# Kernel optimization log

Hardware: AMD Instinct MI355X
Metric: run time of the kernel (lower is better)

The kernel has to match this reference:

```python
import jax, jax.numpy as jnp
import numpy as np

B, S = 4, 2048
DM, H, DK, DV, DI = 512, 4, 128, 128, 1024
NT, NV = 64, 5000
PAD = 0


def layernorm(x, g, b, eps=1e-5):
    m = jnp.mean(x, axis=-1, keepdims=True)
    v = jnp.var(x, axis=-1, keepdims=True)
    return (x - m) * jax.lax.rsqrt(v + eps) * g + b


def setup_inputs() -> dict:
    key = jax.random.key(0)
    ks = jax.random.split(key, 20)
    event_type = jax.random.randint(ks[0], (B, S), 0, NT + 1)
    vertex = jax.random.randint(ks[1], (B, S), 0, NV + 1)
    vertex = jnp.where(event_type == PAD, 0, vertex)  # align padding
    event_time = jnp.sort(jax.random.uniform(ks[2], (B, S)) * 100.0, axis=1)
    non_pad_mask = (event_type != PAD).astype(jnp.float32)[..., None]  # [B,S,1]
    sc = 0.02
    event_emb = jax.random.normal(ks[3], (NT + 1, DM)) * sc
    event_emb = event_emb.at[PAD].set(0.0)
    vertex_emb = jax.random.normal(ks[4], (NV + 1, DM)) * sc
    vertex_emb = vertex_emb.at[PAD].set(0.0)
    A = jax.random.uniform(ks[5], (NV, NV))
    W = jax.random.uniform(ks[6], (NV, NV))
    Wq = jax.random.normal(ks[7], (DM, H * DK)) * sc
    Wk = jax.random.normal(ks[8], (DM, H * DK)) * sc
    Wv = jax.random.normal(ks[9], (DM, H * DV)) * sc
    Wo = jax.random.normal(ks[10], (H * DV, DM)) * sc
    bo = jnp.zeros((DM,))
    ln1_g, ln1_b = jnp.ones((DM,)), jnp.zeros((DM,))
    w1 = jax.random.normal(ks[11], (DM, DI)) * sc
    b1 = jnp.zeros((DI,))
    w2 = jax.random.normal(ks[12], (DI, DM)) * sc
    b2 = jnp.zeros((DM,))
    ln2_g, ln2_b = jnp.ones((DM,)), jnp.zeros((DM,))
    return dict(event_type=event_type, vertex=vertex, event_time=event_time,
                non_pad_mask=non_pad_mask, A=A, W=W, event_emb=event_emb,
                vertex_emb=vertex_emb, Wq=Wq, Wk=Wk, Wv=Wv, Wo=Wo, bo=bo,
                ln1_g=ln1_g, ln1_b=ln1_b, w1=w1, b1=b1, w2=w2, b2=b2,
                ln2_g=ln2_g, ln2_b=ln2_b)


def similarity(vertex, A, W):
    # vectorized form of the triple-loop pairwise gather: [B,1,S,S]
    idx = jnp.clip(vertex - 1, 0)                       # [B,S]
    vm = (vertex != 0)
    pair = vm[:, :, None] & vm[:, None, :]              # [B,S,S]
    sim = A[idx[:, :, None], idx[:, None, :]] * W[idx[:, :, None], idx[:, None, :]] * 10.0
    return (sim * pair.astype(A.dtype))[:, None]        # [B,1,S,S]


def temporal_enc(event_time, non_pad_mask, d_model):
    i = jnp.arange(d_model)
    pv = jnp.power(jnp.float32(10000.0), 2.0 * (i // 2).astype(jnp.float32) / d_model)
    r = event_time[:, :, None] / pv                     # [B,S,D]
    return jnp.where(i % 2 == 0, jnp.sin(r), jnp.cos(r)) * non_pad_mask


def reference(event_type, vertex, event_time, non_pad_mask, A, W, event_emb,
              vertex_emb, Wq, Wk, Wv, Wo, bo, ln1_g, ln1_b, w1, b1, w2, b2,
              ln2_g, ln2_b):
    b_, s_ = event_type.shape
    # masks: key-padding OR subsequent (causal)
    pad = (event_type == PAD)
    subseq = jnp.triu(jnp.ones((s_, s_), dtype=bool), 1)
    slf_attn_mask = pad[:, None, :] | subseq[None]      # [B,S,S]

    sim = similarity(vertex, A, W)                      # [B,1,S,S]
    tem = temporal_enc(event_time, non_pad_mask, DM)    # [B,S,D]
    ver = vertex_emb[vertex]                            # [B,S,D]
    enc = event_emb[event_type]                         # [B,S,D]

    # single encoder layer (n_layers=1), post-norm THP-style
    enc = enc + ver + tem
    res = enc
    q = (enc @ Wq).reshape(b_, s_, H, DK)
    k = (enc @ Wk).reshape(b_, s_, H, DK)
    v = (enc @ Wv).reshape(b_, s_, H, DV)
    scores = jnp.einsum('bihd,bjhd->bhij', q, k) / jnp.sqrt(jnp.float32(DK)) + sim
    scores = jnp.where(slf_attn_mask[:, None], jnp.float32(-1e9), scores)
    attn = jax.nn.softmax(scores, axis=-1)
    o = jnp.einsum('bhij,bjhd->bihd', attn, v).reshape(b_, s_, H * DV)
    o = o @ Wo + bo
    enc = layernorm(o + res, ln1_g, ln1_b) * non_pad_mask
    res = enc
    f = jax.nn.relu(enc @ w1 + b1) @ w2 + b2
    enc = layernorm(f + res, ln2_g, ln2_b) * non_pad_mask
    return enc, sim
```

## Files before the change

### kernel.cpp

```cpp
#include <hip/hip_runtime.h>
#include <hip/hip_bf16.h>

#define B_ 4
#define S_ 2048
#define DM_ 512
#define H_ 4
#define DK_ 128
#define DI_ 1024
#define NV_ 5000

typedef __attribute__((ext_vector_type(8))) short bf16x8;
typedef __attribute__((ext_vector_type(8))) unsigned short u16x8;
typedef __attribute__((ext_vector_type(4))) unsigned short u16x4;
typedef __attribute__((ext_vector_type(4))) float f32x4;

__device__ inline unsigned short f2bf(float x) {
  unsigned int u = __float_as_uint(x);
  unsigned int r = (u + 0x7fffu + ((u >> 16) & 1u)) >> 16;
  return (unsigned short)r;
}
__device__ inline float bf2f(unsigned short u) {
  return __uint_as_float(((unsigned int)u) << 16);
}
__device__ inline void gload16(const void* g, void* l) {
  __builtin_amdgcn_global_load_lds(
      (const __attribute__((address_space(1))) void*)g,
      (__attribute__((address_space(3))) void*)l, 16, 0, 0);
}

__global__ __launch_bounds__(256) void embed_kernel(
    const int* __restrict__ et, const int* __restrict__ vx,
    const float* __restrict__ tmv, const float* __restrict__ npm,
    const float* __restrict__ eemb, const float* __restrict__ vemb,
    float* __restrict__ enc0, unsigned short* __restrict__ enc0b) {
  int row = blockIdx.x;
  int t = et[row], v = vx[row];
  float time = tmv[row], mask = npm[row];
  int tid = threadIdx.x;
  #pragma unroll
  for (int k = 0; k < 2; ++k) {
    int dd = tid + k * 256;
    float pv = powf(10000.0f, (float)(dd & ~1) / 512.0f);
    float r = time / pv;
    float tem = (((dd & 1) == 0) ? sinf(r) : cosf(r)) * mask;
    float val = eemb[(size_t)t * DM_ + dd] + vemb[(size_t)v * DM_ + dd] + tem;
    enc0[(size_t)row * DM_ + dd] = val;
    enc0b[(size_t)row * DM_ + dd] = f2bf(val);
  }
}

__global__ __launch_bounds__(256) void sim_kernel(
    const int* __restrict__ vx, const float* __restrict__ A,
    const float* __restrict__ W, float* __restrict__ sim) {
  __shared__ float Ar[NV_];
  __shared__ float Wr[NV_];
  int i = blockIdx.x;
  int b = blockIdx.y;
  int vi = vx[b * S_ + i];
  float* out = sim + ((size_t)(b * S_ + i)) * S_;
  int tid = threadIdx.x;
  if (vi == 0) {
    for (int j = tid * 4; j < S_; j += 1024)
      *(float4*)&out[j] = (float4){0.f, 0.f, 0.f, 0.f};
    return;
  }
  const float4* Arow = (const float4*)(A + (size_t)(vi - 1) * NV_);
  const float4* Wrow = (const float4*)(W + (size_t)(vi - 1) * NV_);
  for (int j = tid; j < NV_ / 4; j += 256) {
    ((float4*)Ar)[j] = Arow[j];
    ((float4*)Wr)[j] = Wrow[j];
  }
  __syncthreads();
  for (int j = tid * 4; j < S_; j += 1024) {
    int4 vj = *(const int4*)&vx[b * S_ + j];
    float4 o;
    o.x = vj.x ? Ar[vj.x - 1] * Wr[vj.x - 1] * 10.0f : 0.f;
    o.y = vj.y ? Ar[vj.y - 1] * Wr[vj.y - 1] * 10.0f : 0.f;
    o.z = vj.z ? Ar[vj.z - 1] * Wr[vj.z - 1] * 10.0f : 0.f;
    o.w = vj.w ? Ar[vj.w - 1] * Wr[vj.w - 1] * 10.0f : 0.f;
    *(float4*)&out[j] = o;
  }
}

__global__ __launch_bounds__(256) void wt_kernel(
    const float* __restrict__ W, unsigned short* __restrict__ WT,
    int K, int N) {
  __shared__ unsigned short T[32][40];
  int n0 = blockIdx.x * 32, k0 = blockIdx.y * 32;
  int r = threadIdx.x >> 3, c0 = (threadIdx.x & 7) * 4;
  float4 v = *(const float4*)&W[(size_t)(k0 + r) * N + n0 + c0];
  T[r][c0 + 0] = f2bf(v.x);
  T[r][c0 + 1] = f2bf(v.y);
  T[r][c0 + 2] = f2bf(v.z);
  T[r][c0 + 3] = f2bf(v.w);
  __syncthreads();
  u16x4 o;
  o[0] = T[c0 + 0][r]; o[1] = T[c0 + 1][r];
  o[2] = T[c0 + 2][r]; o[3] = T[c0 + 3][r];
  *(u16x4*)&WT[(size_t)(n0 + r) * K + k0 + c0] = o;
}

template <int OMODE, bool RELU>
__global__ __launch_bounds__(256) void gemm_bf16_kernel(
    const unsigned short* __restrict__ A, const unsigned short* __restrict__ BT,
    const float* __restrict__ bias, void* __restrict__ C,
    int M, int N, int K) {
  __shared__ __attribute__((aligned(16))) unsigned short As[128][72];
  __shared__ __attribute__((aligned(16))) unsigned short Bs[128][72];
  int tid = threadIdx.x;
  int w = tid >> 6, l = tid & 63;
  int l16 = l & 15, lh = l >> 4;
  int wr = w >> 1, wc = w & 1;
  int row0 = blockIdx.y * 128, col0 = blockIdx.x * 128;
  int ra = tid >> 1, ha = (tid & 1) * 32;
  f32x4 acc[4][4];
  #pragma unroll
  for (int m = 0; m < 4; ++m)
    #pragma unroll
    for (int n = 0; n < 4; ++n) acc[m][n] = (f32x4){0.f, 0.f, 0.f, 0.f};

  for (int k0 = 0; k0 < K; k0 += 64) {
    __syncthreads();
    {
      const unsigned short* sa = &A[(size_t)(row0 + ra) * K + k0 + ha];
      uint4 a0 = *(const uint4*)(sa);
      uint4 a1 = *(const uint4*)(sa + 8);
      uint4 a2 = *(const uint4*)(sa + 16);
      uint4 a3 = *(const uint4*)(sa + 24);
      *(uint4*)&As[ra][ha + 0] = a0;
      *(uint4*)&As[ra][ha + 8] = a1;
      *(uint4*)&As[ra][ha + 16] = a2;
      *(uint4*)&As[ra][ha + 24] = a3;
      const unsigned short* sb = &BT[(size_t)(col0 + ra) * K + k0 + ha];
      uint4 b0 = *(const uint4*)(sb);
      uint4 b1 = *(const uint4*)(sb + 8);
      uint4 b2 = *(const uint4*)(sb + 16);
      uint4 b3 = *(const uint4*)(sb + 24);
      *(uint4*)&Bs[ra][ha + 0] = b0;
      *(uint4*)&Bs[ra][ha + 8] = b1;
      *(uint4*)&Bs[ra][ha + 16] = b2;
      *(uint4*)&Bs[ra][ha + 24] = b3;
    }
    __syncthreads();
    #pragma unroll
    for (int kc = 0; kc < 2; ++kc) {
      bf16x8 af[4], bfr[4];
      #pragma unroll
      for (int m = 0; m < 4; ++m)
        af[m] = *(bf16x8*)&As[wr * 64 + m * 16 + l16][kc * 32 + lh * 8];
      #pragma unroll
      for (int n = 0; n < 4; ++n)
        bfr[n] = *(bf16x8*)&Bs[wc * 64 + n * 16 + l16][kc * 32 + lh * 8];
      #pragma unroll
      for (int m = 0; m < 4; ++m)
        #pragma unroll
        for (int n = 0; n < 4; ++n)
          acc[m][n] = __builtin_amdgcn_mfma_f32_16x16x32_bf16(af[m], bfr[n], acc[m][n], 0, 0, 0);
    }
  }
  #pragma unroll
  for (int m = 0; m < 4; ++m) {
    #pragma unroll
    for (int r = 0; r < 4; ++r) {
      int row = row0 + wr * 64 + m * 16 + lh * 4 + r;
      #pragma unroll
      for (int n = 0; n < 4; ++n) {
        int colg = col0 + wc * 64 + n * 16 + l16;
        float v = acc[m][n][r];
        if (bias) v += bias[colg];
        if (RELU) v = fmaxf(v, 0.f);
        if (OMODE == 0) {
          ((float*)C)[(size_t)row * N + colg] = v;
        } else if (OMODE == 1) {
          ((unsigned short*)C)[(size_t)row * N + colg] = f2bf(v);
        } else {
          int which = colg >> 9;
          int cl = colg & 511;
          int b = row >> 11, s = row & 2047;
          int h = cl >> 7, d = cl & 127;
          unsigned short* base =
              (unsigned short*)C + (size_t)which * (4194304);
          if (which < 2)
            base[((size_t)((b * 4 + h) * 2048 + s)) * 128 + d] = f2bf(v);
          else
            base[((size_t)((b * 4 + h) * 128 + d)) * 2048 + s] = f2bf(v);
        }
      }
    }
  }
}

__global__ __launch_bounds__(256) void attn_mfma_kernel(
    const unsigned short* __restrict__ Qb, const unsigned short* __restrict__ Kb,
    const unsigned short* __restrict__ Vt, const float* __restrict__ sim,
    const float* __restrict__ npm, unsigned short* __restrict__ Op0,
    unsigned short* __restrict__ Op1, float2* __restrict__ ml0,
    float2* __restrict__ ml1) {
  __shared__ __attribute__((aligned(16))) char KsL[2][16384];
  __shared__ __attribute__((aligned(16))) char VtsL[2][16384];
  __shared__ __attribute__((aligned(16))) unsigned short Pl[4][16][72];
  int bid = blockIdx.x;
  int xcd = bid & 7;
  int j0 = bid >> 3;
  int bh = xcd * 2 + (j0 & 1);
  int jj = j0 >> 1;
  int pair = jj & 15;
  int half = jj >> 4;
  int b = bh >> 2;
  int tid = threadIdx.x;
  int w = tid >> 6, l = tid & 63;
  int l16 = l & 15, lh = l >> 4;
  unsigned short* Op = half ? Op1 : Op0;
  float2* ml = half ? ml1 : ml0;

  const char* KbB = (const char*)Kb + (size_t)bh * 2048 * 256;
  const char* VtB = (const char*)Vt + (size_t)bh * 128 * 4096;
  int krow[4], kcol[4], vrow4[4], vcol[4];
  #pragma unroll
  for (int j = 0; j < 4; ++j) {
    int i = w * 4 + j;
    krow[j] = i * 4 + (l >> 4);
    kcol[j] = ((l & 15) * 16) ^ ((krow[j] & 7) << 4);
    vrow4[j] = i * 8 + (l >> 3);
    vcol[j] = ((l & 7) * 16) ^ ((vrow4[j] & 7) << 4);
  }
  int xr = (l16 & 7) << 4;

  #pragma unroll 1
  for (int pj = 0; pj < 2; ++pj) {
    int qt = pj ? 31 - pair : pair;
    int nst = qt + 1;
    int c0 = (nst + 1) >> 1;
    int t0 = half ? c0 : 0;
    int cnt = half ? nst - c0 : c0;
    int q0 = qt * 64 + w * 16;
    int qg = q0 + l16;

    bf16x8 qf[4];
    const unsigned short* Qrow = Qb + ((size_t)(bh * 2048 + qg)) * 128;
    #pragma unroll
    for (int kq = 0; kq < 4; ++kq)
      qf[kq] = *(const bf16x8*)&Qrow[kq * 32 + lh * 8];

    float m_l = -INFINITY, l_l = 0.f;
    f32x4 o_acc[8];
    #pragma unroll
    for (int c = 0; c < 8; ++c) o_acc[c] = (f32x4){0.f, 0.f, 0.f, 0.f};

    const float* simrow = sim + ((size_t)(b * 2048) + qg) * 2048;
    const float* mrow = npm + b * 2048;

    if (cnt > 0) {
      #pragma unroll
      for (int j = 0; j < 4; ++j) {
        int i = w * 4 + j;
        gload16(KbB + (size_t)(t0 * 64 + krow[j]) * 256 + kcol[j],
                &KsL[0][i * 1024]);
        gload16(VtB + (size_t)vrow4[j] * 4096 + (size_t)(t0 * 64) * 2 + vcol[j],
                &VtsL[0][i * 1024]);
      }
      asm volatile("s_waitcnt vmcnt(0)" ::: "memory");
      __syncthreads();

      #pragma unroll 1
      for (int ti = 0; ti < cnt; ++ti) {
        int cur = ti & 1;
        int kv0 = (t0 + ti) * 64;
        if (ti + 1 < cnt) {
          int kvn = kv0 + 64;
          #pragma unroll
          for (int j = 0; j < 4; ++j) {
            int i = w * 4 + j;
            gload16(KbB + (size_t)(kvn + krow[j]) * 256 + kcol[j],
                    &KsL[cur ^ 1][i * 1024]);
            gload16(VtB + (size_t)vrow4[j] * 4096 + (size_t)kvn * 2 + vcol[j],
                    &VtsL[cur ^ 1][i * 1024]);
          }
        }
        const char* Kbase = KsL[cur];
        f32x4 sc[4];
        #pragma unroll
        for (int tt = 0; tt < 4; ++tt) {
          sc[tt] = (f32x4){0.f, 0.f, 0.f, 0.f};
          const char* Krow = Kbase + (tt * 16 + l16) * 256;
          #pragma unroll
          for (int kq = 0; kq < 4; ++kq) {
            bf16x8 kf = *(const bf16x8*)(Krow + ((kq * 64 + lh * 16) ^ xr));
            sc[tt] = __builtin_amdgcn_mfma_f32_16x16x32_bf16(kf, qf[kq], sc[tt], 0, 0, 0);
          }
        }
        float4 sim4[4], mk4[4];
        #pragma unroll
        for (int tt = 0; tt < 4; ++tt) {
          sim4[tt] = *(const float4*)&simrow[kv0 + tt * 16 + lh * 4];
          mk4[tt] = *(const float4*)&mrow[kv0 + tt * 16 + lh * 4];
        }
        float sv[4][4];
        #pragma unroll
        for (int tt = 0; tt < 4; ++tt) {
          #pragma unroll
          for (int r = 0; r < 4; ++r) {
            int kvg = kv0 + tt * 16 + lh * 4 + r;
            float mkr = r == 0 ? mk4[tt].x : r == 1 ? mk4[tt].y
                      : r == 2 ? mk4[tt].z : mk4[tt].w;
            float smr = r == 0 ? sim4[tt].x : r == 1 ? sim4[tt].y
                      : r == 2 ? sim4[tt].z : sim4[tt].w;
            bool valid = (kvg <= qg) && (mkr != 0.f);
            sv[tt][r] = valid ? sc[tt][r] * 0.08838834764831845f + smr : -1e9f;
          }
        }
        float mx = sv[0][0];
        #pragma unroll
        for (int tt = 0; tt < 4; ++tt)
          #pragma unroll
          for (int r = 0; r < 4; ++r) mx = fmaxf(mx, sv[tt][r]);
        mx = fmaxf(mx, __shfl_xor(mx, 16));
        mx = fmaxf(mx, __shfl_xor(mx, 32));
        float mn = fmaxf(m_l, mx);
        float alpha = __expf(m_l - mn);
        m_l = mn;
        float ts = 0.f;
        #pragma unroll
        for (int tt = 0; tt < 4; ++tt)
          #pragma unroll
          for (int r = 0; r < 4; ++r) {
            float ppv = __expf(sv[tt][r] - mn);
            sv[tt][r] = ppv;
            ts += ppv;
          }
        ts += __shfl_xor(ts, 16);
        ts += __shfl_xor(ts, 32);
        l_l = l_l * alpha + ts;
        #pragma unroll
        for (int tt = 0; tt < 4; ++tt) {
          u16x4 pw;
          pw[0] = f2bf(sv[tt][0]); pw[1] = f2bf(sv[tt][1]);
          pw[2] = f2bf(sv[tt][2]); pw[3] = f2bf(sv[tt][3]);
          *(u16x4*)&Pl[w][l16][tt * 16 + lh * 4] = pw;
        }
        float al[4];
        #pragma unroll
        for (int r = 0; r < 4; ++r) al[r] = __shfl(alpha, lh * 4 + r);
        #pragma unroll
        for (int c = 0; c < 8; ++c)
          #pragma unroll
          for (int r = 0; r < 4; ++r) o_acc[c][r] *= al[r];
        const char* Vbase = VtsL[cur];
        #pragma unroll
        for (int kf2 = 0; kf2 < 2; ++kf2) {
          bf16x8 pa = *(bf16x8*)&Pl[w][l16][kf2 * 32 + lh * 8];
          #pragma unroll
          for (int c = 0; c < 8; ++c) {
            bf16x8 vf = *(const bf16x8*)(Vbase + (c * 16 + l16) * 128 +
                                         ((kf2 * 64 + lh * 16) ^ xr));
            o_acc[c] = __builtin_amdgcn_mfma_f32_16x16x32_bf16(pa, vf, o_acc[c], 0, 0, 0);
          }
        }
        asm volatile("s_waitcnt vmcnt(0)" ::: "memory");
        __syncthreads();
      }
    }
    #pragma unroll
    for (int r = 0; r < 4; ++r) {
      int qgr = q0 + lh * 4 + r;
      unsigned short* op = Op + ((size_t)(bh * 2048 + qgr)) * 128;
      #pragma unroll
      for (int c = 0; c < 8; ++c) op[c * 16 + l16] = f2bf(o_acc[c][r]);
    }
    if (lh == 0) {
      float2 v; v.x = m_l; v.y = l_l;
      ml[bh * 2048 + q0 + l16] = v;
    }
    __syncthreads();
  }
}

__global__ __launch_bounds__(256) void attn_combine_kernel(
    const unsigned short* __restrict__ Op0, const unsigned short* __restrict__ Op1,
    const float2* __restrict__ ml0, const float2* __restrict__ ml1,
    unsigned short* __restrict__ Of) {
  int idx = blockIdx.x * 256 + threadIdx.x;
  int row = idx >> 4;
  int d0 = (idx & 15) * 8;
  float2 a = ml0[row], c2 = ml1[row];
  float m = fmaxf(a.x, c2.x);
  float e1 = __expf(a.x - m), e2 = __expf(c2.x - m);
  float inv = 1.f / (e1 * a.y + e2 * c2.y);
  u16x8 o1 = *(const u16x8*)&Op0[(size_t)row * 128 + d0];
  u16x8 o2 = *(const u16x8*)&Op1[(size_t)row * 128 + d0];
  int bh = row >> 11, q = row & 2047;
  int b = bh >> 2, h = bh & 3;
  unsigned short* dst = Of + ((size_t)(b * 2048 + q)) * 512 + h * 128 + d0;
  u16x8 o;
  #pragma unroll
  for (int j = 0; j < 8; ++j)
    o[j] = f2bf((bf2f(o1[j]) * e1 + bf2f(o2[j]) * e2) * inv);
  *(u16x8*)dst = o;
}

__global__ __launch_bounds__(256) void ln_kernel(
    const float* __restrict__ x, const float* __restrict__ res,
    const float* __restrict__ g, const float* __restrict__ bta,
    const float* __restrict__ npm, float* __restrict__ out,
    unsigned short* __restrict__ out16) {
  __shared__ float ssum[4], ssq[4];
  int row = blockIdx.x;
  int tid = threadIdx.x;
  size_t base = (size_t)row * DM_;
  float v0 = x[base + tid] + res[base + tid];
  float v1 = x[base + tid + 256] + res[base + tid + 256];
  float sum = v0 + v1, sq = v0 * v0 + v1 * v1;
  #pragma unroll
  for (int off = 32; off >= 1; off >>= 1) {
    sum += __shfl_down(sum, off);
    sq += __shfl_down(sq, off);
  }
  int wid = tid >> 6, lane = tid & 63;
  if (lane == 0) { ssum[wid] = sum; ssq[wid] = sq; }
  __syncthreads();
  sum = ssum[0] + ssum[1] + ssum[2] + ssum[3];
  sq = ssq[0] + ssq[1] + ssq[2] + ssq[3];
  float mean = sum * (1.f / DM_);
  float var = sq * (1.f / DM_) - mean * mean;
  float rs = rsqrtf(var + 1e-5f);
  float mask = npm[row];
  float o0 = ((v0 - mean) * rs * g[tid] + bta[tid]) * mask;
  float o1 = ((v1 - mean) * rs * g[tid + 256] + bta[tid + 256]) * mask;
  out[base + tid] = o0;
  out[base + tid + 256] = o1;
  if (out16) {
    out16[base + tid] = f2bf(o0);
    out16[base + tid + 256] = f2bf(o1);
  }
}

extern "C" void kernel_launch(void* const* d_in, const int* in_sizes, int n_in,
                              void* d_out, int out_size, void* d_ws,
                              size_t ws_size, hipStream_t stream) {
  const int* et = (const int*)d_in[0];
  const int* vx = (const int*)d_in[1];
  const float* tmv = (const float*)d_in[2];
  const float* npm = (const float*)d_in[3];
  const float* Amat = (const float*)d_in[4];
  const float* Wmat = (const float*)d_in[5];
  const float* eemb = (const float*)d_in[6];
  const float* vemb = (const float*)d_in[7];
  const float* Wq = (const float*)d_in[8];
  const float* Wk = (const float*)d_in[9];
  const float* Wv = (const float*)d_in[10];
  const float* Wo = (const float*)d_in[11];
  const float* bo = (const float*)d_in[12];
  const float* ln1g = (const float*)d_in[13];
  const float* ln1b = (const float*)d_in[14];
  const float* w1 = (const float*)d_in[15];
  const float* b1 = (const float*)d_in[16];
  const float* w2 = (const float*)d_in[17];
  const float* b2 = (const float*)d_in[18];
  const float* ln2g = (const float*)d_in[19];
  const float* ln2b = (const float*)d_in[20];

  float* out = (float*)d_out;
  float* enc_out = out;
  float* sim_out = out + (size_t)B_ * S_ * DM_;

  const size_t MB = 1ull << 20;
  char* wsb = (char*)d_ws;
  float* enc0 = (float*)(wsb + 0);
  unsigned short* enc0b = (unsigned short*)(wsb + 16 * MB);
  unsigned short* WqT = (unsigned short*)(wsb + 24 * MB);
  unsigned short* WkT = WqT + 512 * 512;
  unsigned short* WvT = WkT + 512 * 512;
  unsigned short* WoT = WvT + 512 * 512;
  unsigned short* w1T = WoT + 512 * 512;
  unsigned short* w2T = w1T + 1024 * 512;
  unsigned short* Qb16 = (unsigned short*)(wsb + 28 * MB);
  unsigned short* Kb16 = (unsigned short*)(wsb + 36 * MB);
  unsigned short* Vt16 = (unsigned short*)(wsb + 44 * MB);
  unsigned short* Op0 = (unsigned short*)(wsb + 52 * MB);
  unsigned short* Op1 = enc0b;
  float2* ml0 = (float2*)(wsb + 60 * MB);
  float2* ml1 = ml0 + 32768;
  unsigned short* Of16 = Qb16;
  float* OP = (float*)(wsb + 88 * MB);
  float* enc1 = OP;
  unsigned short* enc1b = enc0b;
  unsigned short* hid = Kb16;
  float* fbuf = (float*)(wsb + 52 * MB);

  int M = B_ * S_;

  embed_kernel<<<dim3(M), dim3(256), 0, stream>>>(et, vx, tmv, npm, eemb, vemb,
                                                  enc0, enc0b);
  sim_kernel<<<dim3(S_, B_), dim3(256), 0, stream>>>(vx, Amat, Wmat, sim_out);

  wt_kernel<<<dim3(16, 16), dim3(256), 0, stream>>>(Wq, WqT, 512, 512);
  wt_kernel<<<dim3(16, 16), dim3(256), 0, stream>>>(Wk, WkT, 512, 512);
  wt_kernel<<<dim3(16, 16), dim3(256), 0, stream>>>(Wv, WvT, 512, 512);
  wt_kernel<<<dim3(16, 16), dim3(256), 0, stream>>>(Wo, WoT, 512, 512);
  wt_kernel<<<dim3(32, 16), dim3(256), 0, stream>>>(w1, w1T, 512, 1024);
  wt_kernel<<<dim3(16, 32), dim3(256), 0, stream>>>(w2, w2T, 1024, 512);

  gemm_bf16_kernel<5, false><<<dim3(12, 64), dim3(256), 0, stream>>>(
      enc0b, WqT, nullptr, Qb16, M, 3 * DM_, DM_);

  attn_mfma_kernel<<<dim3(512), dim3(256), 0, stream>>>(
      Qb16, Kb16, Vt16, sim_out, npm, Op0, Op1, ml0, ml1);
  attn_combine_kernel<<<dim3(2048), dim3(256), 0, stream>>>(
      Op0, Op1, ml0, ml1, Of16);

  gemm_bf16_kernel<0, false><<<dim3(4, 64), dim3(256), 0, stream>>>(
      Of16, WoT, bo, OP, M, DM_, DM_);
  ln_kernel<<<dim3(M), dim3(256), 0, stream>>>(OP, enc0, ln1g, ln1b, npm, enc1,
                                               enc1b);

  gemm_bf16_kernel<1, true><<<dim3(8, 64), dim3(256), 0, stream>>>(
      enc1b, w1T, b1, hid, M, DI_, DM_);
  gemm_bf16_kernel<0, false><<<dim3(4, 64), dim3(256), 0, stream>>>(
      hid, w2T, b2, fbuf, M, DM_, DI_);
  ln_kernel<<<dim3(M), dim3(256), 0, stream>>>(fbuf, enc1, ln2g, ln2b, npm,
                                               enc_out, nullptr);
}
```

Baseline: 305.1 us.

## Add 64-row GEMM tiles, merge weight transposes, precompute sim products

The output-projection and FFN GEMMs gain a 64-row tile variant, which doubles the grid so more blocks run on the many compute units. The six weight-transpose launches become one kernel. The similarity kernel forms the A*W*10 product once per row in shared memory, so the gather loop does one lookup instead of two loads and two multiplies. The positional encoding swaps powf plus a divide for __expf plus a multiply. Smaller tiles lower per-block reuse, and __expf may shift results slightly.

```diff
diff --git a/kernel.cpp b/kernel.cpp
--- a/kernel.cpp
+++ b/kernel.cpp
@@ -40,8 +40,8 @@
   #pragma unroll
   for (int k = 0; k < 2; ++k) {
     int dd = tid + k * 256;
-    float pv = powf(10000.0f, (float)(dd & ~1) / 512.0f);
-    float r = time / pv;
+    float pvinv = __expf((float)(dd & ~1) * -0.017988946039015984f);
+    float r = time * pvinv;
     float tem = (((dd & 1) == 0) ? sinf(r) : cosf(r)) * mask;
     float val = eemb[(size_t)t * DM_ + dd] + vemb[(size_t)v * DM_ + dd] + tem;
     enc0[(size_t)row * DM_ + dd] = val;
@@ -52,8 +52,7 @@
 __global__ __launch_bounds__(256) void sim_kernel(
     const int* __restrict__ vx, const float* __restrict__ A,
     const float* __restrict__ W, float* __restrict__ sim) {
-  __shared__ float Ar[NV_];
-  __shared__ float Wr[NV_];
+  __shared__ float AWr[NV_];
   int i = blockIdx.x;
   int b = blockIdx.y;
   int vi = vx[b * S_ + i];
@@ -67,28 +66,45 @@
   const float4* Arow = (const float4*)(A + (size_t)(vi - 1) * NV_);
   const float4* Wrow = (const float4*)(W + (size_t)(vi - 1) * NV_);
   for (int j = tid; j < NV_ / 4; j += 256) {
-    ((float4*)Ar)[j] = Arow[j];
-    ((float4*)Wr)[j] = Wrow[j];
+    float4 a = Arow[j];
+    float4 w = Wrow[j];
+    float4 p;
+    p.x = a.x * w.x * 10.0f; p.y = a.y * w.y * 10.0f;
+    p.z = a.z * w.z * 10.0f; p.w = a.w * w.w * 10.0f;
+    ((float4*)AWr)[j] = p;
   }
   __syncthreads();
   for (int j = tid * 4; j < S_; j += 1024) {
     int4 vj = *(const int4*)&vx[b * S_ + j];
     float4 o;
-    o.x = vj.x ? Ar[vj.x - 1] * Wr[vj.x - 1] * 10.0f : 0.f;
-    o.y = vj.y ? Ar[vj.y - 1] * Wr[vj.y - 1] * 10.0f : 0.f;
-    o.z = vj.z ? Ar[vj.z - 1] * Wr[vj.z - 1] * 10.0f : 0.f;
-    o.w = vj.w ? Ar[vj.w - 1] * Wr[vj.w - 1] * 10.0f : 0.f;
+    o.x = vj.x ? AWr[vj.x - 1] : 0.f;
+    o.y = vj.y ? AWr[vj.y - 1] : 0.f;
+    o.z = vj.z ? AWr[vj.z - 1] : 0.f;
+    o.w = vj.w ? AWr[vj.w - 1] : 0.f;
     *(float4*)&out[j] = o;
   }
 }
 
-__global__ __launch_bounds__(256) void wt_kernel(
-    const float* __restrict__ W, unsigned short* __restrict__ WT,
-    int K, int N) {
+__global__ __launch_bounds__(256) void wt_all_kernel(
+    const float* __restrict__ Wq, const float* __restrict__ Wk,
+    const float* __restrict__ Wv, const float* __restrict__ Wo,
+    const float* __restrict__ w1, const float* __restrict__ w2,
+    unsigned short* __restrict__ WqT, unsigned short* __restrict__ WkT,
+    unsigned short* __restrict__ WvT, unsigned short* __restrict__ WoT,
+    unsigned short* __restrict__ w1T, unsigned short* __restrict__ w2T) {
   __shared__ unsigned short T[32][40];
-  int n0 = blockIdx.x * 32, k0 = blockIdx.y * 32;
+  int bid = blockIdx.x;
+  const float* src; unsigned short* dst; int K, N, lid;
+  if (bid < 256)       { src = Wq; dst = WqT; K = 512;  N = 512;  lid = bid; }
+  else if (bid < 512)  { src = Wk; dst = WkT; K = 512;  N = 512;  lid = bid - 256; }
+  else if (bid < 768)  { src = Wv; dst = WvT; K = 512;  N = 512;  lid = bid - 512; }
+  else if (bid < 1024) { src = Wo; dst = WoT; K = 512;  N = 512;  lid = bid - 768; }
+  else if (bid < 1536) { src = w1; dst = w1T; K = 512;  N = 1024; lid = bid - 1024; }
+  else                 { src = w2; dst = w2T; K = 1024; N = 512;  lid = bid - 1536; }
+  int nt = N / 32;
+  int n0 = (lid % nt) * 32, k0 = (lid / nt) * 32;
   int r = threadIdx.x >> 3, c0 = (threadIdx.x & 7) * 4;
-  float4 v = *(const float4*)&W[(size_t)(k0 + r) * N + n0 + c0];
+  float4 v = *(const float4*)&src[(size_t)(k0 + r) * N + n0 + c0];
   T[r][c0 + 0] = f2bf(v.x);
   T[r][c0 + 1] = f2bf(v.y);
   T[r][c0 + 2] = f2bf(v.z);
@@ -97,31 +113,33 @@
   u16x4 o;
   o[0] = T[c0 + 0][r]; o[1] = T[c0 + 1][r];
   o[2] = T[c0 + 2][r]; o[3] = T[c0 + 3][r];
-  *(u16x4*)&WT[(size_t)(n0 + r) * K + k0 + c0] = o;
-}
-
-template <int OMODE, bool RELU>
+  *(u16x4*)&dst[(size_t)(n0 + r) * K + k0 + c0] = o;
+}
+
+template <int OMODE, bool RELU, int MT = 128>
 __global__ __launch_bounds__(256) void gemm_bf16_kernel(
     const unsigned short* __restrict__ A, const unsigned short* __restrict__ BT,
     const float* __restrict__ bias, void* __restrict__ C,
     int M, int N, int K) {
-  __shared__ __attribute__((aligned(16))) unsigned short As[128][72];
+  __shared__ __attribute__((aligned(16))) unsigned short As[MT][72];
   __shared__ __attribute__((aligned(16))) unsigned short Bs[128][72];
   int tid = threadIdx.x;
   int w = tid >> 6, l = tid & 63;
   int l16 = l & 15, lh = l >> 4;
-  int wr = w >> 1, wc = w & 1;
-  int row0 = blockIdx.y * 128, col0 = blockIdx.x * 128;
+  const int NFR = (MT == 128) ? 4 : 2;
+  int wr = (MT == 128) ? (w >> 1) : 0;
+  int wc = (MT == 128) ? (w & 1) : w;
+  int row0 = blockIdx.y * MT, col0 = blockIdx.x * 128;
   int ra = tid >> 1, ha = (tid & 1) * 32;
   f32x4 acc[4][4];
   #pragma unroll
   for (int m = 0; m < 4; ++m)
     #pragma unroll
-    for (int n = 0; n < 4; ++n) acc[m][n] = (f32x4){0.f, 0.f, 0.f, 0.f};
+    for (int n = 0; n < NFR; ++n) acc[m][n] = (f32x4){0.f, 0.f, 0.f, 0.f};
 
   for (int k0 = 0; k0 < K; k0 += 64) {
     __syncthreads();
-    {
+    if (MT == 128) {
       const unsigned short* sa = &A[(size_t)(row0 + ra) * K + k0 + ha];
       uint4 a0 = *(const uint4*)(sa);
       uint4 a1 = *(const uint4*)(sa + 8);
@@ -131,6 +149,15 @@
       *(uint4*)&As[ra][ha + 8] = a1;
       *(uint4*)&As[ra][ha + 16] = a2;
       *(uint4*)&As[ra][ha + 24] = a3;
+    } else {
+      int ra2 = tid >> 2, ha2 = (tid & 3) * 16;
+      const unsigned short* sa = &A[(size_t)(row0 + ra2) * K + k0 + ha2];
+      uint4 a0 = *(const uint4*)(sa);
+      uint4 a1 = *(const uint4*)(sa + 8);
+      *(uint4*)&As[ra2][ha2 + 0] = a0;
+      *(uint4*)&As[ra2][ha2 + 8] = a1;
+    }
+    {
       const unsigned short* sb = &BT[(size_t)(col0 + ra) * K + k0 + ha];
       uint4 b0 = *(const uint4*)(sb);
       uint4 b1 = *(const uint4*)(sb + 8);
@@ -149,12 +176,12 @@
       for (int m = 0; m < 4; ++m)
         af[m] = *(bf16x8*)&As[wr * 64 + m * 16 + l16][kc * 32 + lh * 8];
       #pragma unroll
-      for (int n = 0; n < 4; ++n)
-        bfr[n] = *(bf16x8*)&Bs[wc * 64 + n * 16 + l16][kc * 32 + lh * 8];
+      for (int n = 0; n < NFR; ++n)
+        bfr[n] = *(bf16x8*)&Bs[wc * (16 * NFR) + n * 16 + l16][kc * 32 + lh * 8];
       #pragma unroll
       for (int m = 0; m < 4; ++m)
         #pragma unroll
-        for (int n = 0; n < 4; ++n)
+        for (int n = 0; n < NFR; ++n)
           acc[m][n] = __builtin_amdgcn_mfma_f32_16x16x32_bf16(af[m], bfr[n], acc[m][n], 0, 0, 0);
     }
   }
@@ -164,8 +191,8 @@
     for (int r = 0; r < 4; ++r) {
       int row = row0 + wr * 64 + m * 16 + lh * 4 + r;
       #pragma unroll
-      for (int n = 0; n < 4; ++n) {
-        int colg = col0 + wc * 64 + n * 16 + l16;
+      for (int n = 0; n < NFR; ++n) {
+        int colg = col0 + wc * (16 * NFR) + n * 16 + l16;
         float v = acc[m][n][r];
         if (bias) v += bias[colg];
         if (RELU) v = fmaxf(v, 0.f);
@@ -493,12 +520,8 @@
                                                   enc0, enc0b);
   sim_kernel<<<dim3(S_, B_), dim3(256), 0, stream>>>(vx, Amat, Wmat, sim_out);
 
-  wt_kernel<<<dim3(16, 16), dim3(256), 0, stream>>>(Wq, WqT, 512, 512);
-  wt_kernel<<<dim3(16, 16), dim3(256), 0, stream>>>(Wk, WkT, 512, 512);
-  wt_kernel<<<dim3(16, 16), dim3(256), 0, stream>>>(Wv, WvT, 512, 512);
-  wt_kernel<<<dim3(16, 16), dim3(256), 0, stream>>>(Wo, WoT, 512, 512);
-  wt_kernel<<<dim3(32, 16), dim3(256), 0, stream>>>(w1, w1T, 512, 1024);
-  wt_kernel<<<dim3(16, 32), dim3(256), 0, stream>>>(w2, w2T, 1024, 512);
+  wt_all_kernel<<<dim3(2048), dim3(256), 0, stream>>>(
+      Wq, Wk, Wv, Wo, w1, w2, WqT, WkT, WvT, WoT, w1T, w2T);
 
   gemm_bf16_kernel<5, false><<<dim3(12, 64), dim3(256), 0, stream>>>(
       enc0b, WqT, nullptr, Qb16, M, 3 * DM_, DM_);
@@ -508,14 +531,14 @@
   attn_combine_kernel<<<dim3(2048), dim3(256), 0, stream>>>(
       Op0, Op1, ml0, ml1, Of16);
 
-  gemm_bf16_kernel<0, false><<<dim3(4, 64), dim3(256), 0, stream>>>(
+  gemm_bf16_kernel<0, false, 64><<<dim3(4, 128), dim3(256), 0, stream>>>(
       Of16, WoT, bo, OP, M, DM_, DM_);
   ln_kernel<<<dim3(M), dim3(256), 0, stream>>>(OP, enc0, ln1g, ln1b, npm, enc1,
                                                enc1b);
 
-  gemm_bf16_kernel<1, true><<<dim3(8, 64), dim3(256), 0, stream>>>(
+  gemm_bf16_kernel<1, true, 64><<<dim3(8, 128), dim3(256), 0, stream>>>(
       enc1b, w1T, b1, hid, M, DI_, DM_);
-  gemm_bf16_kernel<0, false><<<dim3(4, 64), dim3(256), 0, stream>>>(
+  gemm_bf16_kernel<0, false, 64><<<dim3(4, 128), dim3(256), 0, stream>>>(
       hid, w2T, b2, fbuf, M, DM_, DI_);
   ln_kernel<<<dim3(M), dim3(256), 0, stream>>>(fbuf, enc1, ln2g, ln2b, npm,
                                                enc_out, nullptr);
```

New measurement: 276.7 us. -9.3%, faster.
